# Kernel tuning notes

Hardware: AMD Instinct MI355X
Metric: run time of the kernel (lower is better)

The kernel has to match this reference:

```python
import jax, jax.numpy as jnp
import numpy as np

S, B, D, H, F = 2048, 2, 1024, 16, 4096
HD = D // H
EPS = 1e-5


def setup_inputs() -> dict:
    key = jax.random.key(0)
    ks = jax.random.split(key, 16)
    sc_d = 1.0 / np.sqrt(D)
    sc_f = 1.0 / np.sqrt(F)
    return {
        "src": jax.random.normal(ks[0], (S, B, D), jnp.float32),
        # attention projections: Linear weights stored as [in, out] (y = x @ W + b)
        "Wq": jax.random.normal(ks[1], (D, D), jnp.float32) * sc_d,
        "bq": jnp.zeros((D,), jnp.float32),
        "Wk": jax.random.normal(ks[2], (D, D), jnp.float32) * sc_d,
        "bk": jnp.zeros((D,), jnp.float32),
        "Wv": jax.random.normal(ks[3], (D, D), jnp.float32) * sc_d,
        "bv": jnp.zeros((D,), jnp.float32),
        "Wo": jax.random.normal(ks[4], (D, D), jnp.float32) * sc_d,
        "bo": jnp.zeros((D,), jnp.float32),
        # norm1
        "g1": jnp.ones((D,), jnp.float32),
        "be1": jnp.zeros((D,), jnp.float32),
        # FFN
        "W1": jax.random.normal(ks[5], (D, F), jnp.float32) * sc_d,
        "bf1": jnp.zeros((F,), jnp.float32),
        "W2": jax.random.normal(ks[6], (F, D), jnp.float32) * sc_f,
        "bf2": jnp.zeros((D,), jnp.float32),
        # norm2
        "g2": jnp.ones((D,), jnp.float32),
        "be2": jnp.zeros((D,), jnp.float32),
    }


def _layernorm(x, g, b):
    m = jnp.mean(x, axis=-1, keepdims=True)
    v = jnp.mean(jnp.square(x - m), axis=-1, keepdims=True)
    return (x - m) * jax.lax.rsqrt(v + EPS) * g + b


def reference(src, Wq, bq, Wk, bk, Wv, bv, Wo, bo, g1, be1, W1, bf1, W2, bf2, g2, be2):
    # --- self attention (dropout_p=0 / eval mode => dropouts are identity) ---
    scaling = float(HD) ** -0.5
    q = (src @ Wq + bq) * scaling            # [S,B,D]
    k = src @ Wk + bk
    v = src @ Wv + bv
    # split heads: torch view(S, B*H, hd) == reshape(S, B, H, hd)
    qh = q.reshape(S, B, H, HD)
    kh = k.reshape(S, B, H, HD)
    vh = v.reshape(S, B, H, HD)
    scores = jnp.einsum("sbhd,tbhd->bhst", qh, kh)      # [B,H,S,S]
    attn = jax.nn.softmax(scores, axis=-1)
    ctx = jnp.einsum("bhst,tbhd->sbhd", attn, vh).reshape(S, B, D)
    attn_out = ctx @ Wo + bo
    # residual + norm1
    x = _layernorm(src + attn_out, g1, be1)
    # FFN (ReLU)
    ff = jax.nn.relu(x @ W1 + bf1) @ W2 + bf2
    # residual + norm2
    return _layernorm(x + ff, g2, be2)
```

## Files before the change

kernel.cpp:

```cpp
#include <hip/hip_runtime.h>
#include <hip/hip_bf16.h>

#define S_  2048
#define B_  2
#define D_  1024
#define H_  16
#define F_  4096
#define HD_ 64
#define NT_ (S_*B_)

typedef __attribute__((ext_vector_type(8))) short short8;
typedef __attribute__((ext_vector_type(4))) short short4v;
typedef __attribute__((ext_vector_type(4))) float f32x4;

#define MFMA16x16x32(a,b,c) __builtin_amdgcn_mfma_f32_16x16x32_bf16((a),(b),(c),0,0,0)

#define AS1C(p) ((const __attribute__((address_space(1))) void*)(p))
#define AS3(p)  ((__attribute__((address_space(3))) void*)(p))

__device__ __forceinline__ short f2b(float f) {
  union { float f; unsigned u; } x; x.f = f;
  unsigned r = x.u + 0x7FFFu + ((x.u >> 16) & 1u);
  return (short)(r >> 16);
}

__device__ __forceinline__ unsigned cvtpk(float a, float b) {
  unsigned r;
  asm("v_cvt_pk_bf16_f32 %0, %1, %2" : "=v"(r) : "v"(a), "v"(b));
  return r;
}
__device__ __forceinline__ float exp2fast(float x) {
  float r;
  asm("v_exp_f32 %0, %1" : "=v"(r) : "v"(x));
  return r;
}

__global__ __launch_bounds__(256) void to_bf16_k(const float* __restrict__ in,
                                                 short* __restrict__ out) {
  int i = (blockIdx.x * 256 + threadIdx.x) * 8;
  float4 a = *(const float4*)(in + i);
  float4 b = *(const float4*)(in + i + 4);
  short8 o;
  o[0] = f2b(a.x); o[1] = f2b(a.y); o[2] = f2b(a.z); o[3] = f2b(a.w);
  o[4] = f2b(b.x); o[5] = f2b(b.y); o[6] = f2b(b.z); o[7] = f2b(b.w);
  *(short8*)(out + i) = o;
}

__global__ __launch_bounds__(256) void transpose_to_bf16(const float* __restrict__ W,
                                                         short* __restrict__ Wt,
                                                         int K, int N, int colbase, int outK) {
  __shared__ short t[32][33];
  int tx = threadIdx.x & 31, ty = threadIdx.x >> 5;
  int kbase = blockIdx.y * 32, nbase = blockIdx.x * 32;
#pragma unroll
  for (int yy = 0; yy < 4; ++yy) {
    int kk = ty + yy * 8;
    t[kk][tx] = f2b(W[(size_t)(kbase + kk) * N + nbase + tx]);
  }
  __syncthreads();
#pragma unroll
  for (int yy = 0; yy < 4; ++yy) {
    int nn = ty + yy * 8;
    Wt[(size_t)(nbase + nn + colbase) * outK + kbase + tx] = t[tx][nn];
  }
}

template<int MODE>
__global__ __launch_bounds__(256, 2) void gemm_bt(
    const short* __restrict__ A, const short* __restrict__ Bt,
    int M, int N, int K,
    const float* __restrict__ bias0, const float* __restrict__ bias1,
    const float* __restrict__ bias2,
    const float* __restrict__ resid, float* __restrict__ outf,
    short* __restrict__ outq, short* __restrict__ outk, short* __restrict__ outv) {
  __shared__ __align__(16) short As[128 * 64];
  __shared__ __align__(16) short Bs[128 * 64];
  int tid = threadIdx.x;
  int lane = tid & 63, w = tid >> 6;
  int g = lane >> 4, r = lane & 15;
  int wm = w >> 1, wn = w & 1;
  int row0 = blockIdx.y * 128, col0 = blockIdx.x * 128;

  f32x4 acc[4][4];
#pragma unroll
  for (int m = 0; m < 4; ++m)
#pragma unroll
    for (int n = 0; n < 4; ++n) acc[m][n] = (f32x4){0.f, 0.f, 0.f, 0.f};

  for (int kt = 0; kt < K; kt += 64) {
#pragma unroll
    for (int p = 0; p < 4; ++p) {
      int idx = tid + p * 256;
      int row = idx >> 3, c = idx & 7;
      int scol = ((c ^ (row & 7)) << 3);
      __builtin_amdgcn_global_load_lds(AS1C(A  + (size_t)(row0 + row) * K + kt + scol),
                                       AS3(As + idx * 8), 16, 0, 0);
      __builtin_amdgcn_global_load_lds(AS1C(Bt + (size_t)(col0 + row) * K + kt + scol),
                                       AS3(Bs + idx * 8), 16, 0, 0);
    }
    __syncthreads();
    short8 af[4][2], bfr[4][2];
#pragma unroll
    for (int m = 0; m < 4; ++m)
#pragma unroll
      for (int kk = 0; kk < 2; ++kk) {
        int row = wm * 64 + m * 16 + r;
        af[m][kk] = *(const short8*)(As + row * 64 + (((kk * 4 + g) ^ (r & 7)) << 3));
      }
#pragma unroll
    for (int n = 0; n < 4; ++n)
#pragma unroll
      for (int kk = 0; kk < 2; ++kk) {
        int row = wn * 64 + n * 16 + r;
        bfr[n][kk] = *(const short8*)(Bs + row * 64 + (((kk * 4 + g) ^ (r & 7)) << 3));
      }
#pragma unroll
    for (int m = 0; m < 4; ++m)
#pragma unroll
      for (int n = 0; n < 4; ++n)
#pragma unroll
        for (int kk = 0; kk < 2; ++kk)
          acc[m][n] = MFMA16x16x32(af[m][kk], bfr[n][kk], acc[m][n]);
    __syncthreads();
  }

  int rb = row0 + wm * 64, cb = col0 + wn * 64;
#pragma unroll
  for (int m = 0; m < 4; ++m) {
#pragma unroll
    for (int n = 0; n < 4; ++n) {
#pragma unroll
      for (int j = 0; j < 4; ++j) {
        int row = rb + m * 16 + g * 4 + j;
        int col = cb + n * 16 + r;
        float v = acc[m][n][j];
        if (MODE == 0) {
          int s = row >> 1, b = row & 1;
          if (col < 1024) {
            float q = (v + bias0[col]) * (0.125f * 1.44269504088896f);
            int h = col >> 6, hd = col & 63;
            outq[((size_t)(b * H_ + h) * S_ + s) * HD_ + hd] = f2b(q);
          } else if (col < 2048) {
            int c2 = col - 1024;
            float kk = v + bias1[c2];
            int h = c2 >> 6, hd = c2 & 63;
            outk[((size_t)(b * H_ + h) * S_ + s) * HD_ + hd] = f2b(kk);
          } else {
            int c2 = col - 2048;
            float vv = v + bias2[c2];
            int h = c2 >> 6, hd = c2 & 63;
            outv[((size_t)(b * H_ + h) * HD_ + hd) * S_ + s] = f2b(vv);
          }
        } else if (MODE == 1) {
          size_t o = (size_t)row * N + col;
          outf[o] = v + bias0[col] + resid[o];
        } else {
          size_t o = (size_t)row * N + col;
          float t = v + bias0[col];
          outq[o] = f2b(t > 0.f ? t : 0.f);
        }
      }
    }
  }
}

__global__ __launch_bounds__(256, 4) void flash_attn(const short* __restrict__ Q,
                                                     const short* __restrict__ Kb,
                                                     const short* __restrict__ Vt,
                                                     short* __restrict__ ctx) {
  __shared__ __align__(16) short Ks[2][64 * 64];
  __shared__ __align__(16) short Vs[2][64 * 64];
  __shared__ __align__(16) short P[4][16][64];
  int tid = threadIdx.x;
  int lane = tid & 63, w = tid >> 6;
  int g = lane >> 4, r = lane & 15;
  int f = blockIdx.x;
  int xcd = f & 7, loc = f >> 3;
  int bh = xcd * 4 + (loc >> 5);
  int qt = loc & 31;
  const short* qp = Q  + (size_t)bh * S_ * HD_;
  const short* kp = Kb + (size_t)bh * S_ * HD_;
  const short* vp = Vt + (size_t)bh * HD_ * S_;
  int q0 = qt * 64 + w * 16;

  short8 qf[2];
#pragma unroll
  for (int kk = 0; kk < 2; ++kk)
    qf[kk] = *(const short8*)(qp + (size_t)(q0 + r) * HD_ + kk * 32 + g * 8);

  f32x4 acc[4];
  float mi = -1e30f, li = 0.f;
#pragma unroll
  for (int db = 0; db < 4; ++db) acc[db] = (f32x4){0.f, 0.f, 0.f, 0.f};

#pragma unroll
  for (int p = 0; p < 2; ++p) {
    int idx = tid + p * 256;
    int row = idx >> 3, c = idx & 7;
    int scol = ((c ^ (row & 7)) << 3);
    __builtin_amdgcn_global_load_lds(AS1C(kp + (size_t)row * HD_ + scol),
                                     AS3(&Ks[0][0] + idx * 8), 16, 0, 0);
    __builtin_amdgcn_global_load_lds(AS1C(vp + (size_t)row * S_ + scol),
                                     AS3(&Vs[0][0] + idx * 8), 16, 0, 0);
  }
  __syncthreads();

  int cur = 0;
  for (int t = 0; t < S_ / 64; ++t) {
    if (t + 1 < S_ / 64) {
      int kv1 = (t + 1) * 64;
#pragma unroll
      for (int p = 0; p < 2; ++p) {
        int idx = tid + p * 256;
        int row = idx >> 3, c = idx & 7;
        int scol = ((c ^ (row & 7)) << 3);
        __builtin_amdgcn_global_load_lds(AS1C(kp + (size_t)(kv1 + row) * HD_ + scol),
                                         AS3(&Ks[cur ^ 1][0] + idx * 8), 16, 0, 0);
        __builtin_amdgcn_global_load_lds(AS1C(vp + (size_t)row * S_ + kv1 + scol),
                                         AS3(&Vs[cur ^ 1][0] + idx * 8), 16, 0, 0);
      }
    }
    const short* Kc = &Ks[cur][0];
    const short* Vc = &Vs[cur][0];
    short8 kf[4][2];
#pragma unroll
    for (int kb = 0; kb < 4; ++kb)
#pragma unroll
      for (int kk = 0; kk < 2; ++kk) {
        int row = kb * 16 + r;
        kf[kb][kk] = *(const short8*)(Kc + row * 64 + (((kk * 4 + g) ^ (r & 7)) << 3));
      }

    f32x4 st[4];
#pragma unroll
    for (int kb = 0; kb < 4; ++kb) {
      f32x4 tt = (f32x4){0.f, 0.f, 0.f, 0.f};
      tt = MFMA16x16x32(kf[kb][0], qf[0], tt);
      tt = MFMA16x16x32(kf[kb][1], qf[1], tt);
      st[kb] = tt;
    }

    float pm = st[0][0];
#pragma unroll
    for (int kb = 0; kb < 4; ++kb)
#pragma unroll
      for (int j = 0; j < 4; ++j) pm = fmaxf(pm, st[kb][j]);
    pm = fmaxf(pm, __shfl_xor(pm, 16));
    pm = fmaxf(pm, __shfl_xor(pm, 32));
    if (!__all(pm <= mi + 8.0f)) {
      float mn = fmaxf(mi, pm);
      float sc = exp2fast(mi - mn);
      mi = mn;
      li *= sc;
#pragma unroll
      for (int db = 0; db < 4; ++db)
#pragma unroll
        for (int j = 0; j < 4; ++j) acc[db][j] *= sc;
    }
    float rs = 0.f;
#pragma unroll
    for (int kb = 0; kb < 4; ++kb)
#pragma unroll
      for (int j = 0; j < 4; ++j) {
        float p0 = exp2fast(st[kb][j] - mi);
        st[kb][j] = p0;
        rs += p0;
      }
    rs += __shfl_xor(rs, 16);
    rs += __shfl_xor(rs, 32);
    li += rs;

#pragma unroll
    for (int kb = 0; kb < 4; ++kb) {
      unsigned w0 = cvtpk(st[kb][0], st[kb][1]);
      unsigned w1 = cvtpk(st[kb][2], st[kb][3]);
      unsigned long long pw = (unsigned long long)w0 | ((unsigned long long)w1 << 32);
      int col = (kb * 16 + g * 4) ^ ((r & 7) << 3);
      *(unsigned long long*)(&P[w][r][0] + col) = pw;
    }

    short8 vf[4][2];
#pragma unroll
    for (int db = 0; db < 4; ++db)
#pragma unroll
      for (int ks = 0; ks < 2; ++ks) {
        int row = db * 16 + r;
        vf[db][ks] = *(const short8*)(Vc + row * 64 + (((ks * 4 + g) ^ (r & 7)) << 3));
      }
    short8 pf[2];
#pragma unroll
    for (int ks = 0; ks < 2; ++ks) {
      int col = (ks * 32 + g * 8) ^ ((r & 7) << 3);
      pf[ks] = *(const short8*)(&P[w][r][0] + col);
    }

#pragma unroll
    for (int db = 0; db < 4; ++db) {
      acc[db] = MFMA16x16x32(vf[db][0], pf[0], acc[db]);
      acc[db] = MFMA16x16x32(vf[db][1], pf[1], acc[db]);
    }

    __syncthreads();
    cur ^= 1;
  }

  int b = bh >> 4, h = bh & 15;
  float inv = 1.0f / li;
  int s = q0 + r;
  int token = s * B_ + b;
#pragma unroll
  for (int db = 0; db < 4; ++db) {
    unsigned w0 = cvtpk(acc[db][0] * inv, acc[db][1] * inv);
    unsigned w1 = cvtpk(acc[db][2] * inv, acc[db][3] * inv);
    unsigned long long pw = (unsigned long long)w0 | ((unsigned long long)w1 << 32);
    *(unsigned long long*)(ctx + (size_t)token * D_ + h * 64 + db * 16 + g * 4) = pw;
  }
}

__global__ __launch_bounds__(256) void layernorm_k(const float* __restrict__ y,
                                                   const float* __restrict__ gm,
                                                   const float* __restrict__ bt,
                                                   float* __restrict__ of,
                                                   short* __restrict__ ob, int writeb) {
  __shared__ float r1[4], r2[4];
  int row = blockIdx.x, tid = threadIdx.x;
  const float* yr = y + (size_t)row * D_;
  float4 v = *(const float4*)(yr + tid * 4);
  float s1 = v.x + v.y + v.z + v.w;
  float s2 = v.x * v.x + v.y * v.y + v.z * v.z + v.w * v.w;
#pragma unroll
  for (int off = 32; off > 0; off >>= 1) {
    s1 += __shfl_xor(s1, off, 64);
    s2 += __shfl_xor(s2, off, 64);
  }
  int wid = tid >> 6;
  if ((tid & 63) == 0) { r1[wid] = s1; r2[wid] = s2; }
  __syncthreads();
  s1 = r1[0] + r1[1] + r1[2] + r1[3];
  s2 = r2[0] + r2[1] + r2[2] + r2[3];
  float mean = s1 * (1.0f / D_);
  float var = s2 * (1.0f / D_) - mean * mean;
  float rstd = rsqrtf(var + 1e-5f);
  float4 gv = *(const float4*)(gm + tid * 4);
  float4 bv = *(const float4*)(bt + tid * 4);
  float o0 = (v.x - mean) * rstd * gv.x + bv.x;
  float o1 = (v.y - mean) * rstd * gv.y + bv.y;
  float o2 = (v.z - mean) * rstd * gv.z + bv.z;
  float o3 = (v.w - mean) * rstd * gv.w + bv.w;
  float4* op = (float4*)(of + (size_t)row * D_ + tid * 4);
  *op = make_float4(o0, o1, o2, o3);
  if (writeb) {
    short4v o;
    o[0] = f2b(o0); o[1] = f2b(o1); o[2] = f2b(o2); o[3] = f2b(o3);
    *(short4v*)(ob + (size_t)row * D_ + tid * 4) = o;
  }
}

extern "C" void kernel_launch(void* const* d_in, const int* in_sizes, int n_in,
                              void* d_out, int out_size, void* d_ws, size_t ws_size,
                              hipStream_t stream) {
  const float* src = (const float*)d_in[0];
  const float* Wq  = (const float*)d_in[1];
  const float* bq  = (const float*)d_in[2];
  const float* Wk  = (const float*)d_in[3];
  const float* bk  = (const float*)d_in[4];
  const float* Wv  = (const float*)d_in[5];
  const float* bv  = (const float*)d_in[6];
  const float* Wo  = (const float*)d_in[7];
  const float* bo  = (const float*)d_in[8];
  const float* g1  = (const float*)d_in[9];
  const float* be1 = (const float*)d_in[10];
  const float* W1  = (const float*)d_in[11];
  const float* bf1 = (const float*)d_in[12];
  const float* W2  = (const float*)d_in[13];
  const float* bf2 = (const float*)d_in[14];
  const float* g2  = (const float*)d_in[15];
  const float* be2 = (const float*)d_in[16];
  float* out = (float*)d_out;
  char* ws = (char*)d_ws;

  short* Wqkv_t = (short*)(ws + 0);
  short* Wo_t   = (short*)(ws + 6291456);
  short* W1_t   = (short*)(ws + 8388608);
  short* W2_t   = (short*)(ws + 16777216);
  short* xb     = (short*)(ws + 25165824);
  short* ctx    = (short*)(ws + 33554432);
  float* res1   = (float*)(ws + 41943040);
  short* hid    = (short*)(ws + 25165824);
  short* qb_    = (short*)(ws + 58720256);
  short* kb_    = (short*)(ws + 67108864);
  float* res2   = (float*)(ws + 58720256);
  short* vb_    = (short*)(ws + 75497472);
  float* x1f    = (float*)(ws + 83886080);
  short* x1b    = (short*)(ws + 100663296);

  to_bf16_k<<<2048, 256, 0, stream>>>(src, xb);

  transpose_to_bf16<<<dim3(32, 32),  256, 0, stream>>>(Wq, Wqkv_t, 1024, 1024, 0,    1024);
  transpose_to_bf16<<<dim3(32, 32),  256, 0, stream>>>(Wk, Wqkv_t, 1024, 1024, 1024, 1024);
  transpose_to_bf16<<<dim3(32, 32),  256, 0, stream>>>(Wv, Wqkv_t, 1024, 1024, 2048, 1024);
  transpose_to_bf16<<<dim3(32, 32),  256, 0, stream>>>(Wo, Wo_t,   1024, 1024, 0,    1024);
  transpose_to_bf16<<<dim3(128, 32), 256, 0, stream>>>(W1, W1_t,   1024, 4096, 0,    1024);
  transpose_to_bf16<<<dim3(32, 128), 256, 0, stream>>>(W2, W2_t,   4096, 1024, 0,    4096);

  gemm_bt<0><<<dim3(24, 32), 256, 0, stream>>>(xb, Wqkv_t, NT_, 3072, 1024,
                                               bq, bk, bv, nullptr, nullptr, qb_, kb_, vb_);
  flash_attn<<<1024, 256, 0, stream>>>(qb_, kb_, vb_, ctx);
  gemm_bt<1><<<dim3(8, 32), 256, 0, stream>>>(ctx, Wo_t, NT_, 1024, 1024,
                                              bo, nullptr, nullptr, src, res1,
                                              nullptr, nullptr, nullptr);
  layernorm_k<<<NT_, 256, 0, stream>>>(res1, g1, be1, x1f, x1b, 1);
  gemm_bt<2><<<dim3(32, 32), 256, 0, stream>>>(x1b, W1_t, NT_, 4096, 1024,
                                               bf1, nullptr, nullptr, nullptr, nullptr,
                                               hid, nullptr, nullptr);
  gemm_bt<1><<<dim3(8, 32), 256, 0, stream>>>(hid, W2_t, NT_, 1024, 4096,
                                              bf2, nullptr, nullptr, x1f, res2,
                                              nullptr, nullptr, nullptr);
  layernorm_k<<<NT_, 256, 0, stream>>>(res2, g2, be2, out, nullptr, 0);
}
```

Measured before the change: 268.5 us.

## Split-K the output and FFN-down GEMMs and fuse partial reduction into layernorm

The Wo and W2 GEMMs are split along K into two halves via a grid z dimension, writing fp32 partials. The layernorm kernels now sum both partials plus bias and residual, so the residual epilogue leaves the GEMM. All GEMMs get an XCD-aware block index swizzle. The second residual is read as bf16 instead of fp32, which saves bandwidth but loses precision, and the partial buffers add extra memory traffic.

```diff
diff --git a/kernel.cpp b/kernel.cpp
--- a/kernel.cpp
+++ b/kernel.cpp
@@ -23,7 +23,10 @@
   unsigned r = x.u + 0x7FFFu + ((x.u >> 16) & 1u);
   return (short)(r >> 16);
 }
-
+__device__ __forceinline__ float b2f(short u) {
+  union { unsigned u; float f; } x; x.u = ((unsigned)(unsigned short)u) << 16;
+  return x.f;
+}
 __device__ __forceinline__ unsigned cvtpk(float a, float b) {
   unsigned r;
   asm("v_cvt_pk_bf16_f32 %0, %1, %2" : "=v"(r) : "v"(a), "v"(b));
@@ -68,10 +71,10 @@
 template<int MODE>
 __global__ __launch_bounds__(256, 2) void gemm_bt(
     const short* __restrict__ A, const short* __restrict__ Bt,
-    int M, int N, int K,
+    int M, int N, int K, int lda,
     const float* __restrict__ bias0, const float* __restrict__ bias1,
     const float* __restrict__ bias2,
-    const float* __restrict__ resid, float* __restrict__ outf,
+    float* __restrict__ outf,
     short* __restrict__ outq, short* __restrict__ outk, short* __restrict__ outv) {
   __shared__ __align__(16) short As[128 * 64];
   __shared__ __align__(16) short Bs[128 * 64];
@@ -79,7 +82,17 @@
   int lane = tid & 63, w = tid >> 6;
   int g = lane >> 4, r = lane & 15;
   int wm = w >> 1, wn = w & 1;
-  int row0 = blockIdx.y * 128, col0 = blockIdx.x * 128;
+
+  int gx = gridDim.x, gy = gridDim.y;
+  int nwg = gx * gy * gridDim.z;
+  int flat = (blockIdx.z * gy + blockIdx.y) * gx + blockIdx.x;
+  int cpx = nwg >> 3;
+  int swz = (flat & 7) * cpx + (flat >> 3);
+  int z = swz / (gx * gy);
+  int rem = swz - z * gx * gy;
+  int row0 = (rem / gx) * 128;
+  int col0 = (rem % gx) * 128;
+  size_t koff = (size_t)z * K;
 
   f32x4 acc[4][4];
 #pragma unroll
@@ -93,9 +106,9 @@
       int idx = tid + p * 256;
       int row = idx >> 3, c = idx & 7;
       int scol = ((c ^ (row & 7)) << 3);
-      __builtin_amdgcn_global_load_lds(AS1C(A  + (size_t)(row0 + row) * K + kt + scol),
+      __builtin_amdgcn_global_load_lds(AS1C(A  + (size_t)(row0 + row) * lda + koff + kt + scol),
                                        AS3(As + idx * 8), 16, 0, 0);
-      __builtin_amdgcn_global_load_lds(AS1C(Bt + (size_t)(col0 + row) * K + kt + scol),
+      __builtin_amdgcn_global_load_lds(AS1C(Bt + (size_t)(col0 + row) * lda + koff + kt + scol),
                                        AS3(Bs + idx * 8), 16, 0, 0);
     }
     __syncthreads();
@@ -151,13 +164,12 @@
             int h = c2 >> 6, hd = c2 & 63;
             outv[((size_t)(b * H_ + h) * HD_ + hd) * S_ + s] = f2b(vv);
           }
-        } else if (MODE == 1) {
-          size_t o = (size_t)row * N + col;
-          outf[o] = v + bias0[col] + resid[o];
-        } else {
+        } else if (MODE == 2) {
           size_t o = (size_t)row * N + col;
           float t = v + bias0[col];
           outq[o] = f2b(t > 0.f ? t : 0.f);
+        } else {
+          outf[(size_t)z * M * N + (size_t)row * N + col] = v;
         }
       }
     }
@@ -317,15 +329,33 @@
   }
 }
 
-__global__ __launch_bounds__(256) void layernorm_k(const float* __restrict__ y,
-                                                   const float* __restrict__ gm,
-                                                   const float* __restrict__ bt,
-                                                   float* __restrict__ of,
-                                                   short* __restrict__ ob, int writeb) {
+template<int RESBF16, int WF, int WB>
+__global__ __launch_bounds__(256) void layernorm_fused(
+    const float* __restrict__ p0, const float* __restrict__ p1,
+    const float* __restrict__ bias,
+    const float* __restrict__ residf, const short* __restrict__ residb,
+    const float* __restrict__ gm, const float* __restrict__ bt,
+    float* __restrict__ of, short* __restrict__ ob) {
   __shared__ float r1[4], r2[4];
   int row = blockIdx.x, tid = threadIdx.x;
-  const float* yr = y + (size_t)row * D_;
-  float4 v = *(const float4*)(yr + tid * 4);
+  size_t base = (size_t)row * D_ + tid * 4;
+  float4 a = *(const float4*)(p0 + base);
+  float4 b = *(const float4*)(p1 + base);
+  float4 bi = *(const float4*)(bias + tid * 4);
+  float4 v;
+  if (RESBF16) {
+    short4v rb = *(const short4v*)(residb + base);
+    v.x = a.x + b.x + bi.x + b2f(rb[0]);
+    v.y = a.y + b.y + bi.y + b2f(rb[1]);
+    v.z = a.z + b.z + bi.z + b2f(rb[2]);
+    v.w = a.w + b.w + bi.w + b2f(rb[3]);
+  } else {
+    float4 rf = *(const float4*)(residf + base);
+    v.x = a.x + b.x + bi.x + rf.x;
+    v.y = a.y + b.y + bi.y + rf.y;
+    v.z = a.z + b.z + bi.z + rf.z;
+    v.w = a.w + b.w + bi.w + rf.w;
+  }
   float s1 = v.x + v.y + v.z + v.w;
   float s2 = v.x * v.x + v.y * v.y + v.z * v.z + v.w * v.w;
 #pragma unroll
@@ -347,12 +377,11 @@
   float o1 = (v.y - mean) * rstd * gv.y + bv.y;
   float o2 = (v.z - mean) * rstd * gv.z + bv.z;
   float o3 = (v.w - mean) * rstd * gv.w + bv.w;
-  float4* op = (float4*)(of + (size_t)row * D_ + tid * 4);
-  *op = make_float4(o0, o1, o2, o3);
-  if (writeb) {
+  if (WF) *(float4*)(of + base) = make_float4(o0, o1, o2, o3);
+  if (WB) {
     short4v o;
     o[0] = f2b(o0); o[1] = f2b(o1); o[2] = f2b(o2); o[3] = f2b(o3);
-    *(short4v*)(ob + (size_t)row * D_ + tid * 4) = o;
+    *(short4v*)(ob + base) = o;
   }
 }
 
@@ -379,20 +408,20 @@
   float* out = (float*)d_out;
   char* ws = (char*)d_ws;
 
-  short* Wqkv_t = (short*)(ws + 0);
-  short* Wo_t   = (short*)(ws + 6291456);
-  short* W1_t   = (short*)(ws + 8388608);
-  short* W2_t   = (short*)(ws + 16777216);
-  short* xb     = (short*)(ws + 25165824);
-  short* ctx    = (short*)(ws + 33554432);
-  float* res1   = (float*)(ws + 41943040);
-  short* hid    = (short*)(ws + 25165824);
-  short* qb_    = (short*)(ws + 58720256);
-  short* kb_    = (short*)(ws + 67108864);
-  float* res2   = (float*)(ws + 58720256);
-  short* vb_    = (short*)(ws + 75497472);
-  float* x1f    = (float*)(ws + 83886080);
-  short* x1b    = (short*)(ws + 100663296);
+  const size_t MiB = 1024 * 1024;
+  short* Wqkv_t = (short*)(ws + 0 * MiB);
+  short* Wo_t   = (short*)(ws + 6 * MiB);
+  short* W1_t   = (short*)(ws + 8 * MiB);
+  short* W2_t   = (short*)(ws + 16 * MiB);
+  short* xb     = (short*)(ws + 24 * MiB);
+  short* x1b    = (short*)(ws + 24 * MiB);
+  short* ctx    = (short*)(ws + 32 * MiB);
+  short* qb_    = (short*)(ws + 40 * MiB);
+  short* kb_    = (short*)(ws + 48 * MiB);
+  short* vb_    = (short*)(ws + 56 * MiB);
+  short* hid    = (short*)(ws + 32 * MiB);
+  float* part   = (float*)(ws + 64 * MiB);
+  float* part1  = part + (size_t)NT_ * D_;
 
   to_bf16_k<<<2048, 256, 0, stream>>>(src, xb);
 
@@ -403,18 +432,20 @@
   transpose_to_bf16<<<dim3(128, 32), 256, 0, stream>>>(W1, W1_t,   1024, 4096, 0,    1024);
   transpose_to_bf16<<<dim3(32, 128), 256, 0, stream>>>(W2, W2_t,   4096, 1024, 0,    4096);
 
-  gemm_bt<0><<<dim3(24, 32), 256, 0, stream>>>(xb, Wqkv_t, NT_, 3072, 1024,
-                                               bq, bk, bv, nullptr, nullptr, qb_, kb_, vb_);
+  gemm_bt<0><<<dim3(24, 32, 1), 256, 0, stream>>>(xb, Wqkv_t, NT_, 3072, 1024, 1024,
+                                                  bq, bk, bv, nullptr, qb_, kb_, vb_);
   flash_attn<<<1024, 256, 0, stream>>>(qb_, kb_, vb_, ctx);
-  gemm_bt<1><<<dim3(8, 32), 256, 0, stream>>>(ctx, Wo_t, NT_, 1024, 1024,
-                                              bo, nullptr, nullptr, src, res1,
-                                              nullptr, nullptr, nullptr);
-  layernorm_k<<<NT_, 256, 0, stream>>>(res1, g1, be1, x1f, x1b, 1);
-  gemm_bt<2><<<dim3(32, 32), 256, 0, stream>>>(x1b, W1_t, NT_, 4096, 1024,
-                                               bf1, nullptr, nullptr, nullptr, nullptr,
-                                               hid, nullptr, nullptr);
-  gemm_bt<1><<<dim3(8, 32), 256, 0, stream>>>(hid, W2_t, NT_, 1024, 4096,
-                                              bf2, nullptr, nullptr, x1f, res2,
-                                              nullptr, nullptr, nullptr);
-  layernorm_k<<<NT_, 256, 0, stream>>>(res2, g2, be2, out, nullptr, 0);
-}
+  gemm_bt<3><<<dim3(8, 32, 2), 256, 0, stream>>>(ctx, Wo_t, NT_, 1024, 512, 1024,
+                                                 nullptr, nullptr, nullptr, part,
+                                                 nullptr, nullptr, nullptr);
+  layernorm_fused<0, 0, 1><<<NT_, 256, 0, stream>>>(part, part1, bo, src, nullptr,
+                                                    g1, be1, nullptr, x1b);
+  gemm_bt<2><<<dim3(32, 32, 1), 256, 0, stream>>>(x1b, W1_t, NT_, 4096, 1024, 1024,
+                                                  bf1, nullptr, nullptr, nullptr,
+                                                  hid, nullptr, nullptr);
+  gemm_bt<3><<<dim3(8, 32, 2), 256, 0, stream>>>(hid, W2_t, NT_, 1024, 2048, 4096,
+                                                 nullptr, nullptr, nullptr, part,
+                                                 nullptr, nullptr, nullptr);
+  layernorm_fused<1, 1, 0><<<NT_, 256, 0, stream>>>(part, part1, bf2, nullptr, x1b,
+                                                    g2, be2, out, nullptr);
+}
```

Measured after the change: 240.2 us. -10.5%, faster.
